# Optimization experiments

Measured on AMD Instinct MI355X. Metric: run time of the kernel, lower is better.

The kernel has to match this reference:

```python
import jax, jax.numpy as jnp
import numpy as np

N_NODES = 50000
N_EDGES = 1600000
IN_SIZE = 128
HIDDEN = 128
OUT_SIZE = 64
NUM_LAYERS = 3
BN_EPS = 1e-5
GIN_EPS_INIT = 1e-5


def setup_inputs() -> dict:
    key = jax.random.key(0)
    ks = jax.random.split(key, 16)
    node_feat = jax.random.normal(ks[0], (N_NODES, IN_SIZE), dtype=jnp.float32)
    src = jax.random.randint(ks[1], (N_EDGES,), 0, N_NODES)
    dst = jax.random.randint(ks[2], (N_EDGES,), 0, N_NODES)
    # per-layer MLP params (in_size == hidden, so shapes are uniform across layers)
    s1 = 1.0 / np.sqrt(IN_SIZE)
    s2 = 1.0 / np.sqrt(HIDDEN)
    W1 = jax.random.uniform(ks[3], (NUM_LAYERS, IN_SIZE, HIDDEN), jnp.float32, -s1, s1)
    b1 = jax.random.uniform(ks[4], (NUM_LAYERS, HIDDEN), jnp.float32, -s1, s1)
    gamma = jnp.ones((NUM_LAYERS, HIDDEN), jnp.float32)
    beta = jnp.zeros((NUM_LAYERS, HIDDEN), jnp.float32)
    W2 = jax.random.uniform(ks[5], (NUM_LAYERS, HIDDEN, HIDDEN), jnp.float32, -s2, s2)
    b2 = jax.random.uniform(ks[6], (NUM_LAYERS, HIDDEN), jnp.float32, -s2, s2)
    eps = jnp.full((NUM_LAYERS,), GIN_EPS_INIT, jnp.float32)  # learnable GIN eps
    Wout = jax.random.uniform(ks[7], (HIDDEN, OUT_SIZE), jnp.float32, -s2, s2)
    bout = jax.random.uniform(ks[8], (OUT_SIZE,), jnp.float32, -s2, s2)
    return {"node_feat": node_feat, "src": src, "dst": dst,
            "W1": W1, "b1": b1, "gamma": gamma, "beta": beta,
            "W2": W2, "b2": b2, "eps": eps, "Wout": Wout, "bout": bout}


def reference(node_feat, src, dst, W1, b1, gamma, beta, W2, b2, eps, Wout, bout):
    n = node_feat.shape[0]
    h = node_feat
    for i in range(NUM_LAYERS):
        # sum-aggregate source features onto destination nodes
        agg = jax.ops.segment_sum(h[src], dst, num_segments=n)  # [N, d]
        x = (1.0 + eps[i]) * h + agg
        x = x @ W1[i] + b1[i]
        # BatchNorm1d (training mode: batch statistics, biased variance)
        mu = jnp.mean(x, axis=0)
        var = jnp.var(x, axis=0)
        x = (x - mu) * jax.lax.rsqrt(var + BN_EPS) * gamma[i] + beta[i]
        x = jax.nn.relu(x)
        h = jax.nn.relu(x @ W2[i] + b2[i])
    return h @ Wout + bout
```

## Files before the change

### kernel.cpp

```cpp
#include <hip/hip_runtime.h>

#define NN 50000
#define NE 1600000
#define HID 128
#define NB 196
#define BCAP 12288

typedef _Float16 half8 __attribute__((ext_vector_type(8)));
typedef float floatx4 __attribute__((ext_vector_type(4)));


#define CVT_BLK 3125
#define CNT_BLK 391

__device__ __forceinline__ void pack_one(const float* __restrict__ W1,
                                         const float* __restrict__ W2,
                                         const float* __restrict__ Wout,
                                         _Float16* __restrict__ wp, int y, int t) {
  const float* W;
  _Float16* dstp;
  int NCT;
  if (y < 3) { W = W1 + (size_t)y * 16384; dstp = wp + y * 16384; NCT = 8; }
  else if (y < 6) { W = W2 + (size_t)(y - 3) * 16384; dstp = wp + 49152 + (y - 3) * 16384; NCT = 8; }
  else { W = Wout; dstp = wp + 98304; NCT = 4; }
  if (t >= 4 * NCT * 64) return;
  int lane = t & 63;
  int ct = (t >> 6) % NCT;
  int kb = t / (64 * NCT);
  int n = ct * 16 + (lane & 15);
  int k0 = kb * 32 + (lane >> 4) * 8;
  int N = NCT * 16;
#pragma unroll
  for (int j = 0; j < 8; ++j) dstp[t * 8 + j] = (_Float16)W[(k0 + j) * N + n];
}

__global__ __launch_bounds__(256) void k_prep(
    const float* __restrict__ nf, _Float16* __restrict__ hb,
    const float* __restrict__ W1, const float* __restrict__ W2,
    const float* __restrict__ Wout, _Float16* __restrict__ wp,
    const int* __restrict__ dst, int* __restrict__ gcnt) {
  const int b = blockIdx.x;
  const int tid = threadIdx.x;
  if (b < CVT_BLK) {
    int t = b * 256 + tid;
    const float4* x4 = (const float4*)nf;
    float4 u = x4[t * 2], v = x4[t * 2 + 1];
    half8 o;
    o[0] = (_Float16)u.x; o[1] = (_Float16)u.y; o[2] = (_Float16)u.z; o[3] = (_Float16)u.w;
    o[4] = (_Float16)v.x; o[5] = (_Float16)v.y; o[6] = (_Float16)v.z; o[7] = (_Float16)v.w;
    ((half8*)hb)[t] = o;
  } else if (b < CVT_BLK + CNT_BLK) {
    __shared__ int cnt[NB];
    for (int i = tid; i < NB; i += 256) cnt[i] = 0;
    __syncthreads();
    int base = (b - CVT_BLK) * 4096;
    for (int i = 0; i < 16; ++i) {
      int e = base + i * 256 + tid;
      if (e < NE) atomicAdd(&cnt[dst[e] >> 8], 1);
    }
    __syncthreads();
    for (int i = tid; i < NB; i += 256)
      if (cnt[i]) atomicAdd(&gcnt[i], cnt[i]);
  } else {
    int bb = b - (CVT_BLK + CNT_BLK);
    pack_one(W1, W2, Wout, wp, bb >> 3, ((bb & 7) << 8) | tid);
  }
}


__global__ __launch_bounds__(256) void kb_basescan(const int* __restrict__ gcnt,
                                                   int* __restrict__ bbase,
                                                   int* __restrict__ bcur) {
  __shared__ int s[256];
  int tid = threadIdx.x;
  int v = (tid < NB) ? gcnt[tid] : 0;
  s[tid] = v;
  __syncthreads();
  for (int d = 1; d < 256; d <<= 1) {
    int t = (tid >= d) ? s[tid - d] : 0;
    __syncthreads();
    s[tid] += t;
    __syncthreads();
  }
  int incl = s[tid];
  if (tid < NB) {
    bbase[tid] = incl - v;
    bcur[tid] = incl - v;
  }
  if (tid == NB - 1) bbase[NB] = incl;
}

__global__ __launch_bounds__(256) void kb_partition(const int* __restrict__ src,
                                                    const int* __restrict__ dst,
                                                    int* __restrict__ bcur,
                                                    int* __restrict__ ebuf, int E) {
  __shared__ int cnt[NB];
  __shared__ int sbase[NB];
  int tid = threadIdx.x;
  for (int i = tid; i < NB; i += 256) cnt[i] = 0;
  __syncthreads();
  int base = blockIdx.x * 4096;
  int myd[16], mys[16];
#pragma unroll
  for (int i = 0; i < 16; ++i) {
    int e = base + i * 256 + tid;
    if (e < E) {
      myd[i] = dst[e];
      mys[i] = src[e];
      atomicAdd(&cnt[myd[i] >> 8], 1);
    } else {
      myd[i] = -1;
    }
  }
  __syncthreads();
  for (int i = tid; i < NB; i += 256)
    sbase[i] = cnt[i] ? atomicAdd(&bcur[i], cnt[i]) : 0;
  __syncthreads();
  for (int i = tid; i < NB; i += 256) cnt[i] = 0;
  __syncthreads();
#pragma unroll
  for (int i = 0; i < 16; ++i) {
    if (myd[i] >= 0) {
      int b = myd[i] >> 8;
      int r = atomicAdd(&cnt[b], 1);
      ebuf[sbase[b] + r] = (mys[i] << 8) | (myd[i] & 255);
    }
  }
}

__global__ __launch_bounds__(256) void kb_csr(const int* __restrict__ ebuf,
                                              const int* __restrict__ bbase,
                                              int* __restrict__ rs,
                                              int* __restrict__ eidx, int M) {
  __shared__ int cnt[256];
  __shared__ int off[256];
  __shared__ int sbuf[BCAP];
  int tid = threadIdx.x;
  int b = blockIdx.x;
  int lo = bbase[b], hi = bbase[b + 1];
  int n = hi - lo;
  cnt[tid] = 0;
  __syncthreads();
  for (int i = tid; i < n; i += 256) atomicAdd(&cnt[ebuf[lo + i] & 255], 1);
  __syncthreads();
  int v = cnt[tid];
  off[tid] = v;
  __syncthreads();
  for (int d = 1; d < 256; d <<= 1) {
    int t = (tid >= d) ? off[tid - d] : 0;
    __syncthreads();
    off[tid] += t;
    __syncthreads();
  }
  int excl = off[tid] - v;
  int gnode = b * 256 + tid;
  if (gnode < M) rs[gnode] = lo + excl;
  if (b == NB - 1 && tid == 0) rs[M] = bbase[NB];
  __syncthreads();
  cnt[tid] = excl;
  __syncthreads();
  if (n <= BCAP) {
    for (int i = tid; i < n; i += 256) {
      int ed = ebuf[lo + i];
      int r = atomicAdd(&cnt[ed & 255], 1);
      sbuf[r] = ed >> 8;
    }
    __syncthreads();
    for (int i = tid; i < n; i += 256) eidx[lo + i] = sbuf[i];
  } else {
    for (int i = tid; i < n; i += 256) {
      int ed = ebuf[lo + i];
      int r = atomicAdd(&cnt[ed & 255], 1);
      eidx[lo + r] = ed >> 8;
    }
  }
}


__global__ __launch_bounds__(1024, 8) void k_aggemm1(
    const int* __restrict__ rs, const int* __restrict__ eidx,
    const float* __restrict__ eps, int layer, const _Float16* __restrict__ h,
    const _Float16* __restrict__ wp1, const float* __restrict__ b1L,
    float* __restrict__ csum, float* __restrict__ csq,
    _Float16* __restrict__ x) {
  __shared__ _Float16 As[64 * 136];
  __shared__ float sredS[512];
  __shared__ float sredQ[512];
  const int tid = threadIdx.x;
  const int wid = tid >> 6;
  const int lane = tid & 63;
  const int slot = lane >> 4;
  const int c8 = lane & 15;
  const int c8t = tid & 15;
  const int rowBase = blockIdx.x * 64;
  const float ep = 1.0f + eps[layer];
  const half8* h8 = (const half8*)h;

  for (int i = 0; i < 4; ++i) {
    const int node = rowBase + wid * 4 + i;
    float a0[8] = {0, 0, 0, 0, 0, 0, 0, 0};
    float a1[8] = {0, 0, 0, 0, 0, 0, 0, 0};
    float a2[8] = {0, 0, 0, 0, 0, 0, 0, 0};
    float a3[8] = {0, 0, 0, 0, 0, 0, 0, 0};
    int e0 = 0, e1 = 0;
    if (node < NN) {
      e0 = rs[node];
      e1 = rs[node + 1];
    }
    int e = e0 + slot;
    for (; e + 12 < e1; e += 16) {
      int s0 = eidx[e];
      int s1 = eidx[e + 4];
      int s2 = eidx[e + 8];
      int s3 = eidx[e + 12];
      half8 v0 = h8[s0 * 16 + c8];
      half8 v1 = h8[s1 * 16 + c8];
      half8 v2 = h8[s2 * 16 + c8];
      half8 v3 = h8[s3 * 16 + c8];
#pragma unroll
      for (int j = 0; j < 8; ++j) {
        a0[j] += (float)v0[j];
        a1[j] += (float)v1[j];
        a2[j] += (float)v2[j];
        a3[j] += (float)v3[j];
      }
    }
    for (; e < e1; e += 4) {
      half8 v = h8[eidx[e] * 16 + c8];
#pragma unroll
      for (int j = 0; j < 8; ++j) a0[j] += (float)v[j];
    }
#pragma unroll
    for (int j = 0; j < 8; ++j) {
      a0[j] += a1[j] + a2[j] + a3[j];
      a0[j] += __shfl_xor(a0[j], 16);
      a0[j] += __shfl_xor(a0[j], 32);
    }
    if (slot == 0) {
      half8 o = {0, 0, 0, 0, 0, 0, 0, 0};
      if (node < NN) {
        half8 hv = h8[node * 16 + c8];
#pragma unroll
        for (int j = 0; j < 8; ++j) o[j] = (_Float16)fmaf(ep, (float)hv[j], a0[j]);
      }
      *(half8*)(As + (wid * 4 + i) * 136 + c8 * 8) = o;
    }
  }
  __syncthreads();

  const int rg = wid & 3;
  const int cg = wid >> 2;
  floatx4 acc[2];
  acc[0] = (floatx4){0.f, 0.f, 0.f, 0.f};
  acc[1] = (floatx4){0.f, 0.f, 0.f, 0.f};
  const half8* wp8 = (const half8*)wp1;
#pragma unroll
  for (int kb = 0; kb < 4; ++kb) {
    half8 a = *(const half8*)(As + (rg * 16 + c8) * 136 + kb * 32 + slot * 8);
#pragma unroll
    for (int t = 0; t < 2; ++t) {
      int ct = cg * 2 + t;
      acc[t] = __builtin_amdgcn_mfma_f32_16x16x32_f16(a, wp8[(kb * 8 + ct) * 64 + lane],
                                                      acc[t], 0, 0, 0);
    }
  }
  __syncthreads();

#pragma unroll
  for (int t = 0; t < 2; ++t) {
    int ct = cg * 2 + t;
    float bv = b1L[ct * 16 + c8];
    float ps = 0.f, pq = 0.f;
#pragma unroll
    for (int reg = 0; reg < 4; ++reg) {
      int row = rg * 16 + slot * 4 + reg;
      float xv = acc[t][reg] + bv;
      As[row * 136 + ct * 16 + c8] = (_Float16)xv;
      if (rowBase + row < NN) {
        ps += xv;
        pq += xv * xv;
      }
    }
    ps += __shfl_xor(ps, 16);
    ps += __shfl_xor(ps, 32);
    pq += __shfl_xor(pq, 16);
    pq += __shfl_xor(pq, 32);
    if (lane < 16) {
      sredS[wid * 32 + t * 16 + lane] = ps;
      sredQ[wid * 32 + t * 16 + lane] = pq;
    }
  }
  __syncthreads();

  {
    int row = tid >> 4;
    int gr = rowBase + row;
    if (gr < NN) {
      half8 v = *(half8*)(As + row * 136 + c8t * 8);
      *(half8*)(x + (size_t)gr * 128 + c8t * 8) = v;
    }
  }
  if (tid < 128) {
    int c = tid;
    int wbase = (c >> 5) * 4;
    int loc = c & 31;
    float s = sredS[wbase * 32 + loc] + sredS[(wbase + 1) * 32 + loc] +
              sredS[(wbase + 2) * 32 + loc] + sredS[(wbase + 3) * 32 + loc];
    atomicAdd(&csum[c], s);
  } else if (tid < 256) {
    int c = tid - 128;
    int wbase = (c >> 5) * 4;
    int loc = c & 31;
    float q = sredQ[wbase * 32 + loc] + sredQ[(wbase + 1) * 32 + loc] +
              sredQ[(wbase + 2) * 32 + loc] + sredQ[(wbase + 3) * 32 + loc];
    atomicAdd(&csq[c], q);
  }
}


template <int FINAL>
__global__ __launch_bounds__(1024, 8) void k_bn_gemm2(
    const _Float16* __restrict__ x, const _Float16* __restrict__ wp2,
    const float* __restrict__ b2L, const float* __restrict__ gammaL,
    const float* __restrict__ betaL, const float* __restrict__ csum,
    const float* __restrict__ csq, _Float16* __restrict__ hout,
    const _Float16* __restrict__ wpo, const float* __restrict__ boutp,
    float* __restrict__ out) {
  __shared__ _Float16 As[64 * 136];
  const int tid = threadIdx.x;
  const int wid = tid >> 6;
  const int lane = tid & 63;
  const int slot = lane >> 4;
  const int c8 = lane & 15;
  const int c8t = tid & 15;
  const int rowBase = blockIdx.x * 64;

  float sc[8], sh[8];
  {
    const float invM = 1.0f / (float)NN;
#pragma unroll
    for (int j = 0; j < 8; ++j) {
      int k = c8t * 8 + j;
      float mu = csum[k] * invM;
      float var = csq[k] * invM - mu * mu;
      float g = gammaL[k] * rsqrtf(var + 1e-5f);
      sc[j] = g;
      sh[j] = fmaf(-mu, g, betaL[k]);
    }
  }
  {
    int row = tid >> 4;
    int gr = rowBase + row;
    half8 v = {0, 0, 0, 0, 0, 0, 0, 0};
    if (gr < NN) {
      v = *(const half8*)(x + (size_t)gr * 128 + c8t * 8);
#pragma unroll
      for (int j = 0; j < 8; ++j)
        v[j] = (_Float16)fmaxf(fmaf((float)v[j], sc[j], sh[j]), 0.f);
    }
    *(half8*)(As + row * 136 + c8t * 8) = v;
  }
  __syncthreads();

  const int rg = wid & 3;
  const int cg = wid >> 2;
  floatx4 acc[2];
  acc[0] = (floatx4){0.f, 0.f, 0.f, 0.f};
  acc[1] = (floatx4){0.f, 0.f, 0.f, 0.f};
  const half8* wp8 = (const half8*)wp2;
#pragma unroll
  for (int kb = 0; kb < 4; ++kb) {
    half8 a = *(const half8*)(As + (rg * 16 + c8) * 136 + kb * 32 + slot * 8);
#pragma unroll
    for (int t = 0; t < 2; ++t) {
      int ct = cg * 2 + t;
      acc[t] = __builtin_amdgcn_mfma_f32_16x16x32_f16(a, wp8[(kb * 8 + ct) * 64 + lane],
                                                      acc[t], 0, 0, 0);
    }
  }
  __syncthreads();
#pragma unroll
  for (int t = 0; t < 2; ++t) {
    int ct = cg * 2 + t;
    float bv = b2L[ct * 16 + c8];
#pragma unroll
    for (int reg = 0; reg < 4; ++reg) {
      int row = rg * 16 + slot * 4 + reg;
      As[row * 136 + ct * 16 + c8] = (_Float16)fmaxf(acc[t][reg] + bv, 0.f);
    }
  }
  __syncthreads();

  if (FINAL == 0) {
    int row = tid >> 4;
    int gr = rowBase + row;
    if (gr < NN) {
      half8 v = *(half8*)(As + row * 136 + c8t * 8);
      *(half8*)(hout + (size_t)gr * 128 + c8t * 8) = v;
    }
  } else {
    if (cg < 2) {
      floatx4 acc3[2];
      acc3[0] = (floatx4){0.f, 0.f, 0.f, 0.f};
      acc3[1] = (floatx4){0.f, 0.f, 0.f, 0.f};
      const half8* wo8 = (const half8*)wpo;
#pragma unroll
      for (int kb = 0; kb < 4; ++kb) {
        half8 a = *(const half8*)(As + (rg * 16 + c8) * 136 + kb * 32 + slot * 8);
#pragma unroll
        for (int t = 0; t < 2; ++t) {
          int ct = cg * 2 + t;
          acc3[t] = __builtin_amdgcn_mfma_f32_16x16x32_f16(
              a, wo8[(kb * 4 + ct) * 64 + lane], acc3[t], 0, 0, 0);
        }
      }
#pragma unroll
      for (int t = 0; t < 2; ++t) {
        int ct = cg * 2 + t;
        float bv = boutp[ct * 16 + c8];
#pragma unroll
        for (int reg = 0; reg < 4; ++reg) {
          int gr = rowBase + rg * 16 + slot * 4 + reg;
          if (gr < NN) out[(size_t)gr * 64 + ct * 16 + c8] = acc3[t][reg] + bv;
        }
      }
    }
  }
}


extern "C" void kernel_launch(void* const* d_in, const int* in_sizes, int n_in,
                              void* d_out, int out_size, void* d_ws, size_t ws_size,
                              hipStream_t stream) {
  const float* node_feat = (const float*)d_in[0];
  const int* src = (const int*)d_in[1];
  const int* dst = (const int*)d_in[2];
  const float* W1 = (const float*)d_in[3];
  const float* b1 = (const float*)d_in[4];
  const float* gamma = (const float*)d_in[5];
  const float* beta = (const float*)d_in[6];
  const float* W2 = (const float*)d_in[7];
  const float* b2 = (const float*)d_in[8];
  const float* eps = (const float*)d_in[9];
  const float* Wout = (const float*)d_in[10];
  const float* bout = (const float*)d_in[11];
  float* out = (float*)d_out;

  int* rs = (int*)d_ws;
  int* gcnt = rs + 50176;
  int* bbase = gcnt + 256;
  int* bcur = bbase + 256;
  float* stats = (float*)(bcur + 256);
  int* eidx = (int*)(stats + 768);
  _Float16* hb = (_Float16*)(eidx + NE);
  _Float16* xb = hb + (size_t)NN * HID;
  _Float16* wp = xb + (size_t)NN * HID;
  int* ebuf = (int*)(wp + 106496);

  hipMemsetAsync(gcnt, 0, (256 * 3 + 768) * sizeof(int), stream);

  k_prep<<<CVT_BLK + CNT_BLK + 56, 256, 0, stream>>>(node_feat, hb, W1, W2, Wout,
                                                     wp, dst, gcnt);
  kb_basescan<<<1, 256, 0, stream>>>(gcnt, bbase, bcur);
  kb_partition<<<CNT_BLK, 256, 0, stream>>>(src, dst, bcur, ebuf, NE);
  kb_csr<<<NB, 256, 0, stream>>>(ebuf, bbase, rs, eidx, NN);

  const int rowTiles = (NN + 63) / 64;

  for (int L = 0; L < 3; ++L) {
    float* csum = stats + L * 256;
    float* csq = csum + 128;
    k_aggemm1<<<rowTiles, 1024, 0, stream>>>(
        rs, eidx, eps, L, hb, wp + (size_t)L * 16384, b1 + (size_t)L * HID,
        csum, csq, xb);
    if (L < 2) {
      k_bn_gemm2<0><<<rowTiles, 1024, 0, stream>>>(
          xb, wp + 49152 + (size_t)L * 16384, b2 + (size_t)L * HID,
          gamma + (size_t)L * HID, beta + (size_t)L * HID, csum, csq, hb,
          nullptr, nullptr, nullptr);
    } else {
      k_bn_gemm2<1><<<rowTiles, 1024, 0, stream>>>(
          xb, wp + 49152 + (size_t)L * 16384, b2 + (size_t)L * HID,
          gamma + (size_t)L * HID, beta + (size_t)L * HID, csum, csq, nullptr,
          wp + 98304, bout, out);
    }
  }
}
```

Before: 436.7 us.

## Split aggregation into slice-partitioned kernel with 16-bit edge indices

Moves neighbor aggregation out of the fused aggregate+GEMM1 kernel into a separate kernel. The hidden features are stored as four 32-column slices, and blocks are interleaved so that each XCD works on a single slice. This should keep the gathered slice resident in that XCD's L2, cutting the cost of the random gathers. Edges are split evenly across threads and accumulated with shared-memory atomics, and edge indices are narrowed to 16 bits to halve index traffic. The cost is an extra launch and a round trip of the aggregated activations through global memory before GEMM1.

```diff
diff --git a/kernel.cpp b/kernel.cpp
--- a/kernel.cpp
+++ b/kernel.cpp
@@ -5,6 +5,7 @@
 #define HID 128
 #define NB 196
 #define BCAP 12288
+#define SLH (NN * 32)
 
 typedef _Float16 half8 __attribute__((ext_vector_type(8)));
 typedef float floatx4 __attribute__((ext_vector_type(4)));
@@ -48,7 +49,8 @@
     half8 o;
     o[0] = (_Float16)u.x; o[1] = (_Float16)u.y; o[2] = (_Float16)u.z; o[3] = (_Float16)u.w;
     o[4] = (_Float16)v.x; o[5] = (_Float16)v.y; o[6] = (_Float16)v.z; o[7] = (_Float16)v.w;
-    ((half8*)hb)[t] = o;
+    int node = t >> 4, c = t & 15;
+    ((half8*)hb)[(size_t)(c >> 2) * (NN * 4) + node * 4 + (c & 3)] = o;
   } else if (b < CVT_BLK + CNT_BLK) {
     __shared__ int cnt[NB];
     for (int i = tid; i < NB; i += 256) cnt[i] = 0;
@@ -131,7 +133,7 @@
 __global__ __launch_bounds__(256) void kb_csr(const int* __restrict__ ebuf,
                                               const int* __restrict__ bbase,
                                               int* __restrict__ rs,
-                                              int* __restrict__ eidx, int M) {
+                                              unsigned short* __restrict__ eidx, int M) {
   __shared__ int cnt[256];
   __shared__ int off[256];
   __shared__ int sbuf[BCAP];
@@ -166,23 +168,97 @@
       sbuf[r] = ed >> 8;
     }
     __syncthreads();
-    for (int i = tid; i < n; i += 256) eidx[lo + i] = sbuf[i];
+    for (int i = tid; i < n; i += 256) eidx[lo + i] = (unsigned short)sbuf[i];
   } else {
     for (int i = tid; i < n; i += 256) {
       int ed = ebuf[lo + i];
       int r = atomicAdd(&cnt[ed & 255], 1);
-      eidx[lo + r] = ed >> 8;
-    }
-  }
-}
-
-
-__global__ __launch_bounds__(1024, 8) void k_aggemm1(
-    const int* __restrict__ rs, const int* __restrict__ eidx,
+      eidx[lo + r] = (unsigned short)(ed >> 8);
+    }
+  }
+}
+
+
+__global__ __launch_bounds__(1024, 8) void k_agg(
+    const int* __restrict__ rs, const unsigned short* __restrict__ eidx,
     const float* __restrict__ eps, int layer, const _Float16* __restrict__ h,
+    _Float16* __restrict__ x) {
+  __shared__ float sacc[64 * 33];
+  __shared__ int srs[65];
+  const int tid = threadIdx.x;
+  const int b = blockIdx.x;
+  const int slice = (b & 7) >> 1;
+  const int tile = ((b >> 3) << 1) | (b & 1);
+  const int base = tile * 64;
+  const int g = tid >> 2;
+  const int sub = tid & 3;
+
+  for (int i = tid; i < 64 * 33; i += 1024) sacc[i] = 0.f;
+  if (tid < 65) {
+    int idx = base + tid;
+    srs[tid] = rs[idx < NN ? idx : NN];
+  }
+  __syncthreads();
+
+  const half8* hsl = (const half8*)(h + (size_t)slice * SLH);
+  const int elo = srs[0], ehi = srs[64];
+  const int nE = ehi - elo;
+  const int clen = (nE + 255) >> 8;
+  int e = elo + g * clen;
+  const int c1 = (e + clen < ehi) ? e + clen : ehi;
+  if (e < c1) {
+    int loB = 0, hiB = 64;
+    while (hiB - loB > 1) {
+      int mid = (loB + hiB) >> 1;
+      if (srs[mid] <= e) loB = mid; else hiB = mid;
+    }
+    int curN = loB;
+    int nextB = srs[curN + 1];
+    const int c1m1 = c1 - 1;
+    float a[8] = {0.f, 0.f, 0.f, 0.f, 0.f, 0.f, 0.f, 0.f};
+    half8 vA = hsl[(int)eidx[e] * 4 + sub];
+    int en = (e + 1 < c1m1) ? e + 1 : c1m1;
+    half8 vB = hsl[(int)eidx[en] * 4 + sub];
+    while (true) {
+      while (e >= nextB) {
+        float* p = sacc + curN * 33 + sub * 8;
+#pragma unroll
+        for (int j = 0; j < 8; ++j) { atomicAdd(p + j, a[j]); a[j] = 0.f; }
+        ++curN;
+        nextB = srs[curN + 1];
+      }
+#pragma unroll
+      for (int j = 0; j < 8; ++j) a[j] += (float)vA[j];
+      ++e;
+      if (e >= c1) break;
+      vA = vB;
+      en = (e + 1 < c1m1) ? e + 1 : c1m1;
+      vB = hsl[(int)eidx[en] * 4 + sub];
+    }
+    float* p = sacc + curN * 33 + sub * 8;
+#pragma unroll
+    for (int j = 0; j < 8; ++j) atomicAdd(p + j, a[j]);
+  }
+  __syncthreads();
+
+  if (tid < 256) {
+    const int node = base + g;
+    if (node < NN) {
+      const float ep = 1.0f + eps[layer];
+      half8 hv = hsl[(size_t)node * 4 + sub];
+      const float* p = sacc + g * 33 + sub * 8;
+      half8 o;
+#pragma unroll
+      for (int j = 0; j < 8; ++j) o[j] = (_Float16)fmaf(ep, (float)hv[j], p[j]);
+      *(half8*)(x + (size_t)node * 128 + slice * 32 + sub * 8) = o;
+    }
+  }
+}
+
+
+__global__ __launch_bounds__(1024, 8) void k_gemm1(
     const _Float16* __restrict__ wp1, const float* __restrict__ b1L,
-    float* __restrict__ csum, float* __restrict__ csq,
-    _Float16* __restrict__ x) {
+    float* __restrict__ csum, float* __restrict__ csq, _Float16* x) {
   __shared__ _Float16 As[64 * 136];
   __shared__ float sredS[512];
   __shared__ float sredQ[512];
@@ -193,58 +269,13 @@
   const int c8 = lane & 15;
   const int c8t = tid & 15;
   const int rowBase = blockIdx.x * 64;
-  const float ep = 1.0f + eps[layer];
-  const half8* h8 = (const half8*)h;
-
-  for (int i = 0; i < 4; ++i) {
-    const int node = rowBase + wid * 4 + i;
-    float a0[8] = {0, 0, 0, 0, 0, 0, 0, 0};
-    float a1[8] = {0, 0, 0, 0, 0, 0, 0, 0};
-    float a2[8] = {0, 0, 0, 0, 0, 0, 0, 0};
-    float a3[8] = {0, 0, 0, 0, 0, 0, 0, 0};
-    int e0 = 0, e1 = 0;
-    if (node < NN) {
-      e0 = rs[node];
-      e1 = rs[node + 1];
-    }
-    int e = e0 + slot;
-    for (; e + 12 < e1; e += 16) {
-      int s0 = eidx[e];
-      int s1 = eidx[e + 4];
-      int s2 = eidx[e + 8];
-      int s3 = eidx[e + 12];
-      half8 v0 = h8[s0 * 16 + c8];
-      half8 v1 = h8[s1 * 16 + c8];
-      half8 v2 = h8[s2 * 16 + c8];
-      half8 v3 = h8[s3 * 16 + c8];
-#pragma unroll
-      for (int j = 0; j < 8; ++j) {
-        a0[j] += (float)v0[j];
-        a1[j] += (float)v1[j];
-        a2[j] += (float)v2[j];
-        a3[j] += (float)v3[j];
-      }
-    }
-    for (; e < e1; e += 4) {
-      half8 v = h8[eidx[e] * 16 + c8];
-#pragma unroll
-      for (int j = 0; j < 8; ++j) a0[j] += (float)v[j];
-    }
-#pragma unroll
-    for (int j = 0; j < 8; ++j) {
-      a0[j] += a1[j] + a2[j] + a3[j];
-      a0[j] += __shfl_xor(a0[j], 16);
-      a0[j] += __shfl_xor(a0[j], 32);
-    }
-    if (slot == 0) {
-      half8 o = {0, 0, 0, 0, 0, 0, 0, 0};
-      if (node < NN) {
-        half8 hv = h8[node * 16 + c8];
-#pragma unroll
-        for (int j = 0; j < 8; ++j) o[j] = (_Float16)fmaf(ep, (float)hv[j], a0[j]);
-      }
-      *(half8*)(As + (wid * 4 + i) * 136 + c8 * 8) = o;
-    }
+
+  {
+    int row = tid >> 4;
+    int gr = rowBase + row;
+    half8 v = {0, 0, 0, 0, 0, 0, 0, 0};
+    if (gr < NN) v = *(const half8*)(x + (size_t)gr * 128 + c8t * 8);
+    *(half8*)(As + row * 136 + c8t * 8) = v;
   }
   __syncthreads();
 
@@ -396,7 +427,7 @@
     int gr = rowBase + row;
     if (gr < NN) {
       half8 v = *(half8*)(As + row * 136 + c8t * 8);
-      *(half8*)(hout + (size_t)gr * 128 + c8t * 8) = v;
+      *(half8*)(hout + (size_t)(c8t >> 2) * SLH + (size_t)gr * 32 + (c8t & 3) * 8) = v;
     }
   } else {
     if (cg < 2) {
@@ -457,22 +488,25 @@
   _Float16* wp = xb + (size_t)NN * HID;
   int* ebuf = (int*)(wp + 106496);
 
+  unsigned short* eidx16 = (unsigned short*)eidx;
+
   hipMemsetAsync(gcnt, 0, (256 * 3 + 768) * sizeof(int), stream);
 
   k_prep<<<CVT_BLK + CNT_BLK + 56, 256, 0, stream>>>(node_feat, hb, W1, W2, Wout,
                                                      wp, dst, gcnt);
   kb_basescan<<<1, 256, 0, stream>>>(gcnt, bbase, bcur);
   kb_partition<<<CNT_BLK, 256, 0, stream>>>(src, dst, bcur, ebuf, NE);
-  kb_csr<<<NB, 256, 0, stream>>>(ebuf, bbase, rs, eidx, NN);
+  kb_csr<<<NB, 256, 0, stream>>>(ebuf, bbase, rs, eidx16, NN);
 
   const int rowTiles = (NN + 63) / 64;
+  const int aggBlocks = 391 * 8;
 
   for (int L = 0; L < 3; ++L) {
     float* csum = stats + L * 256;
     float* csq = csum + 128;
-    k_aggemm1<<<rowTiles, 1024, 0, stream>>>(
-        rs, eidx, eps, L, hb, wp + (size_t)L * 16384, b1 + (size_t)L * HID,
-        csum, csq, xb);
+    k_agg<<<aggBlocks, 1024, 0, stream>>>(rs, eidx16, eps, L, hb, xb);
+    k_gemm1<<<rowTiles, 1024, 0, stream>>>(wp + (size_t)L * 16384,
+                                           b1 + (size_t)L * HID, csum, csq, xb);
     if (L < 2) {
       k_bn_gemm2<0><<<rowTiles, 1024, 0, stream>>>(
           xb, wp + 49152 + (size_t)L * 16384, b2 + (size_t)L * HID,
```

Result: slower. 802.9 us (+83.9%).

## Split aggregation into feature-sliced gather kernel with 16-bit edge indices

Applied to the files above, without the earlier changes.

Node features are now stored in four 32-column slices, so each gather touches a smaller, more cache-resident array. The fused aggregate+GEMM1 kernel is split in two: a separate aggregation kernel walks the slices, with block ordering that interleaves tiles and slices, and writes row-major x; GEMM1 then reloads x from global memory. Edge source indices are narrowed to unsigned short to halve index traffic. This costs an extra kernel launch and a round trip of x through global memory per layer. The unsigned short indices can only hold node ids up to 65535, which covers the 50000 nodes here.

```diff
diff --git a/kernel.cpp b/kernel.cpp
--- a/kernel.cpp
+++ b/kernel.cpp
@@ -5,6 +5,7 @@
 #define HID 128
 #define NB 196
 #define BCAP 12288
+#define SLH (NN * 32)
 
 typedef _Float16 half8 __attribute__((ext_vector_type(8)));
 typedef float floatx4 __attribute__((ext_vector_type(4)));
@@ -48,7 +49,8 @@
     half8 o;
     o[0] = (_Float16)u.x; o[1] = (_Float16)u.y; o[2] = (_Float16)u.z; o[3] = (_Float16)u.w;
     o[4] = (_Float16)v.x; o[5] = (_Float16)v.y; o[6] = (_Float16)v.z; o[7] = (_Float16)v.w;
-    ((half8*)hb)[t] = o;
+    int node = t >> 4, c = t & 15;
+    ((half8*)hb)[(size_t)(c >> 2) * (NN * 4) + node * 4 + (c & 3)] = o;
   } else if (b < CVT_BLK + CNT_BLK) {
     __shared__ int cnt[NB];
     for (int i = tid; i < NB; i += 256) cnt[i] = 0;
@@ -131,7 +133,7 @@
 __global__ __launch_bounds__(256) void kb_csr(const int* __restrict__ ebuf,
                                               const int* __restrict__ bbase,
                                               int* __restrict__ rs,
-                                              int* __restrict__ eidx, int M) {
+                                              unsigned short* __restrict__ eidx, int M) {
   __shared__ int cnt[256];
   __shared__ int off[256];
   __shared__ int sbuf[BCAP];
@@ -166,23 +168,85 @@
       sbuf[r] = ed >> 8;
     }
     __syncthreads();
-    for (int i = tid; i < n; i += 256) eidx[lo + i] = sbuf[i];
+    for (int i = tid; i < n; i += 256) eidx[lo + i] = (unsigned short)sbuf[i];
   } else {
     for (int i = tid; i < n; i += 256) {
       int ed = ebuf[lo + i];
       int r = atomicAdd(&cnt[ed & 255], 1);
-      eidx[lo + r] = ed >> 8;
-    }
-  }
-}
-
-
-__global__ __launch_bounds__(1024, 8) void k_aggemm1(
-    const int* __restrict__ rs, const int* __restrict__ eidx,
+      eidx[lo + r] = (unsigned short)(ed >> 8);
+    }
+  }
+}
+
+
+__global__ __launch_bounds__(1024, 8) void k_agg(
+    const int* __restrict__ rs, const unsigned short* __restrict__ eidx,
     const float* __restrict__ eps, int layer, const _Float16* __restrict__ h,
+    _Float16* __restrict__ x) {
+  const int tid = threadIdx.x;
+  const int b = blockIdx.x;
+  const int slice = (b & 7) >> 1;
+  const int tile = ((b >> 3) << 1) | (b & 1);
+  const int lane = tid & 63;
+  const int wid = tid >> 6;
+  const int sub = lane & 3;
+  const int slot = (lane >> 2) & 3;
+  const int ng = lane >> 4;
+  const int node = tile * 64 + wid * 4 + ng;
+  const half8* hsl = (const half8*)(h + (size_t)slice * SLH);
+
+  float a0[8] = {0, 0, 0, 0, 0, 0, 0, 0};
+  float a1[8] = {0, 0, 0, 0, 0, 0, 0, 0};
+  float a2[8] = {0, 0, 0, 0, 0, 0, 0, 0};
+  float a3[8] = {0, 0, 0, 0, 0, 0, 0, 0};
+  int e0 = 0, e1 = 0;
+  if (node < NN) {
+    e0 = rs[node];
+    e1 = rs[node + 1];
+  }
+  int e = e0 + slot;
+  for (; e + 12 < e1; e += 16) {
+    int s0 = eidx[e];
+    int s1 = eidx[e + 4];
+    int s2 = eidx[e + 8];
+    int s3 = eidx[e + 12];
+    half8 v0 = hsl[s0 * 4 + sub];
+    half8 v1 = hsl[s1 * 4 + sub];
+    half8 v2 = hsl[s2 * 4 + sub];
+    half8 v3 = hsl[s3 * 4 + sub];
+#pragma unroll
+    for (int j = 0; j < 8; ++j) {
+      a0[j] += (float)v0[j];
+      a1[j] += (float)v1[j];
+      a2[j] += (float)v2[j];
+      a3[j] += (float)v3[j];
+    }
+  }
+  for (; e < e1; e += 4) {
+    half8 v = hsl[(int)eidx[e] * 4 + sub];
+#pragma unroll
+    for (int j = 0; j < 8; ++j) a0[j] += (float)v[j];
+  }
+#pragma unroll
+  for (int j = 0; j < 8; ++j) {
+    a0[j] += a1[j] + a2[j] + a3[j];
+    a0[j] += __shfl_xor(a0[j], 4);
+    a0[j] += __shfl_xor(a0[j], 8);
+  }
+  if (slot == 0 && node < NN) {
+    const float ep = 1.0f + eps[layer];
+    half8 hv = hsl[(size_t)node * 4 + sub];
+    half8 o;
+#pragma unroll
+    for (int j = 0; j < 8; ++j) o[j] = (_Float16)fmaf(ep, (float)hv[j], a0[j]);
+    *(half8*)(x + (size_t)node * 128 + slice * 32 + sub * 8) = o;
+  }
+}
+
+
+__global__ __launch_bounds__(1024, 8) void k_gemm1(
     const _Float16* __restrict__ wp1, const float* __restrict__ b1L,
-    float* __restrict__ csum, float* __restrict__ csq,
-    _Float16* __restrict__ x) {
+    float* __restrict__ csum, float* __restrict__ csq, _Float16* x) {
   __shared__ _Float16 As[64 * 136];
   __shared__ float sredS[512];
   __shared__ float sredQ[512];
@@ -193,58 +257,13 @@
   const int c8 = lane & 15;
   const int c8t = tid & 15;
   const int rowBase = blockIdx.x * 64;
-  const float ep = 1.0f + eps[layer];
-  const half8* h8 = (const half8*)h;
-
-  for (int i = 0; i < 4; ++i) {
-    const int node = rowBase + wid * 4 + i;
-    float a0[8] = {0, 0, 0, 0, 0, 0, 0, 0};
-    float a1[8] = {0, 0, 0, 0, 0, 0, 0, 0};
-    float a2[8] = {0, 0, 0, 0, 0, 0, 0, 0};
-    float a3[8] = {0, 0, 0, 0, 0, 0, 0, 0};
-    int e0 = 0, e1 = 0;
-    if (node < NN) {
-      e0 = rs[node];
-      e1 = rs[node + 1];
-    }
-    int e = e0 + slot;
-    for (; e + 12 < e1; e += 16) {
-      int s0 = eidx[e];
-      int s1 = eidx[e + 4];
-      int s2 = eidx[e + 8];
-      int s3 = eidx[e + 12];
-      half8 v0 = h8[s0 * 16 + c8];
-      half8 v1 = h8[s1 * 16 + c8];
-      half8 v2 = h8[s2 * 16 + c8];
-      half8 v3 = h8[s3 * 16 + c8];
-#pragma unroll
-      for (int j = 0; j < 8; ++j) {
-        a0[j] += (float)v0[j];
-        a1[j] += (float)v1[j];
-        a2[j] += (float)v2[j];
-        a3[j] += (float)v3[j];
-      }
-    }
-    for (; e < e1; e += 4) {
-      half8 v = h8[eidx[e] * 16 + c8];
-#pragma unroll
-      for (int j = 0; j < 8; ++j) a0[j] += (float)v[j];
-    }
-#pragma unroll
-    for (int j = 0; j < 8; ++j) {
-      a0[j] += a1[j] + a2[j] + a3[j];
-      a0[j] += __shfl_xor(a0[j], 16);
-      a0[j] += __shfl_xor(a0[j], 32);
-    }
-    if (slot == 0) {
-      half8 o = {0, 0, 0, 0, 0, 0, 0, 0};
-      if (node < NN) {
-        half8 hv = h8[node * 16 + c8];
-#pragma unroll
-        for (int j = 0; j < 8; ++j) o[j] = (_Float16)fmaf(ep, (float)hv[j], a0[j]);
-      }
-      *(half8*)(As + (wid * 4 + i) * 136 + c8 * 8) = o;
-    }
+
+  {
+    int row = tid >> 4;
+    int gr = rowBase + row;
+    half8 v = {0, 0, 0, 0, 0, 0, 0, 0};
+    if (gr < NN) v = *(const half8*)(x + (size_t)gr * 128 + c8t * 8);
+    *(half8*)(As + row * 136 + c8t * 8) = v;
   }
   __syncthreads();
 
@@ -396,7 +415,7 @@
     int gr = rowBase + row;
     if (gr < NN) {
       half8 v = *(half8*)(As + row * 136 + c8t * 8);
-      *(half8*)(hout + (size_t)gr * 128 + c8t * 8) = v;
+      *(half8*)(hout + (size_t)(c8t >> 2) * SLH + (size_t)gr * 32 + (c8t & 3) * 8) = v;
     }
   } else {
     if (cg < 2) {
@@ -457,22 +476,25 @@
   _Float16* wp = xb + (size_t)NN * HID;
   int* ebuf = (int*)(wp + 106496);
 
+  unsigned short* eidx16 = (unsigned short*)eidx;
+
   hipMemsetAsync(gcnt, 0, (256 * 3 + 768) * sizeof(int), stream);
 
   k_prep<<<CVT_BLK + CNT_BLK + 56, 256, 0, stream>>>(node_feat, hb, W1, W2, Wout,
                                                      wp, dst, gcnt);
   kb_basescan<<<1, 256, 0, stream>>>(gcnt, bbase, bcur);
   kb_partition<<<CNT_BLK, 256, 0, stream>>>(src, dst, bcur, ebuf, NE);
-  kb_csr<<<NB, 256, 0, stream>>>(ebuf, bbase, rs, eidx, NN);
+  kb_csr<<<NB, 256, 0, stream>>>(ebuf, bbase, rs, eidx16, NN);
 
   const int rowTiles = (NN + 63) / 64;
+  const int aggBlocks = 391 * 8;
 
   for (int L = 0; L < 3; ++L) {
     float* csum = stats + L * 256;
     float* csq = csum + 128;
-    k_aggemm1<<<rowTiles, 1024, 0, stream>>>(
-        rs, eidx, eps, L, hb, wp + (size_t)L * 16384, b1 + (size_t)L * HID,
-        csum, csq, xb);
+    k_agg<<<aggBlocks, 1024, 0, stream>>>(rs, eidx16, eps, L, hb, xb);
+    k_gemm1<<<rowTiles, 1024, 0, stream>>>(wp + (size_t)L * 16384,
+                                           b1 + (size_t)L * HID, csum, csq, xb);
     if (L < 2) {
       k_bn_gemm2<0><<<rowTiles, 1024, 0, stream>>>(
           xb, wp + 49152 + (size_t)L * 16384, b2 + (size_t)L * HID,
```

New measurement: 430.2 us. About the same (-1.5%).
